# Kernel optimization log

Hardware: AMD Instinct MI355X
Metric: run time of the kernel (lower is better)

## Reference

```python
import jax, jax.numpy as jnp
import numpy as np
import math

D_MODEL = 1024
NUM_HEADS = 16
DK = D_MODEL // NUM_HEADS
THETA = 10000.0


def _rope(x, cos, sin):
    # x: (..., S, dk); cos/sin: (S, dk//2). Interleaved (even/odd) rotation,
    # matching x1=x[...,0::2], x2=x[...,1::2] then re-interleave via stack.
    x1 = x[..., 0::2]
    x2 = x[..., 1::2]
    r1 = x1 * cos - x2 * sin
    r2 = x1 * sin + x2 * cos
    return jnp.stack((r1, r2), axis=-1).reshape(x.shape)


def setup_inputs() -> dict:
    key = jax.random.key(0)
    k1, k2, k3 = jax.random.split(key, 3)
    B, S = 2, 2048
    x = jax.random.normal(k1, (B, S, D_MODEL), dtype=jnp.float32)
    std_qkv = (2.0 / (D_MODEL + 3 * D_MODEL)) ** 0.5
    Wqkv = jax.random.normal(k2, (3 * D_MODEL, D_MODEL), dtype=jnp.float32) * std_qkv
    std_o = (2.0 / (D_MODEL + D_MODEL)) ** 0.5
    Wo = jax.random.normal(k3, (D_MODEL, D_MODEL), dtype=jnp.float32) * std_o
    return {"x": x, "Wqkv": Wqkv, "Wo": Wo}


def reference(x, Wqkv, Wo):
    B, S, D = x.shape
    # fused QKV projection: Linear stores W as (out, in), y = x @ W^T
    qkv = jnp.einsum('bsd,od->bso', x, Wqkv)  # (B, S, 3*D)
    # split order in the source rearrange is (three, numheads, dk)
    qkv = qkv.reshape(B, S, 3, NUM_HEADS, DK).transpose(2, 0, 3, 1, 4)  # (3,B,H,S,dk)
    q, k, v = qkv[0], qkv[1], qkv[2]

    # RoPE tables (registered buffers in the source, deterministic constants)
    inv_freqs = 1.0 / (THETA ** (jnp.arange(0, DK, 2, dtype=jnp.float32) / DK))
    t = jnp.arange(S, dtype=jnp.float32)
    freqs = t[:, None] * inv_freqs[None, :]  # (S, dk//2)
    cos, sin = jnp.cos(freqs), jnp.sin(freqs)
    q = _rope(q, cos, sin)
    k = _rope(k, cos, sin)

    # naive full-materialization causal attention
    scores = jnp.einsum('bhqd,bhkd->bhqk', q, k) / math.sqrt(DK)  # (B,H,S,S)
    causal = jnp.tril(jnp.ones((S, S), dtype=bool))
    scores = jnp.where(causal, scores, -jnp.inf)
    attn = jax.nn.softmax(scores, axis=-1)
    out = jnp.einsum('bhqk,bhkd->bhqd', attn, v)  # (B,H,S,dk)
    out = out.transpose(0, 2, 1, 3).reshape(B, S, D)  # concat heads
    return jnp.einsum('bsd,od->bso', out, Wo)
```

## Files before the change

kernel.cpp:

```cpp
#include <hip/hip_runtime.h>
#include <hip/hip_bf16.h>
#include <cstdint>
#include <cstddef>


typedef unsigned short u16;
typedef unsigned int   u32;

typedef float f32x4 __attribute__((ext_vector_type(4)));
typedef short frag_t __attribute__((ext_vector_type(8)));

__device__ __forceinline__ f32x4 mfma16(frag_t a, frag_t b, f32x4 c) {
  return __builtin_amdgcn_mfma_f32_16x16x32_bf16(a, b, c, 0, 0, 0);
}

typedef __attribute__((address_space(1))) void as1_void;
typedef __attribute__((address_space(3))) void as3_void;
__device__ __forceinline__ void gload_lds16(const void* g, void* l) {
  __builtin_amdgcn_global_load_lds((as1_void*)g, (as3_void*)l, 16, 0, 0);
}

__device__ __forceinline__ u16 f2bf(float f) {
  u32 u = __builtin_bit_cast(u32, f);
  u += 0x7fffu + ((u >> 16) & 1u);
  return (u16)(u >> 16);
}
__device__ __forceinline__ float bf2f(u16 h) {
  u32 u = ((u32)h) << 16;
  return __builtin_bit_cast(float, u);
}
__device__ __forceinline__ u16 bf16u(float f) {
  __hip_bfloat16 h = __float2bfloat16(f);
  u16 u;
  __builtin_memcpy(&u, &h, 2);
  return u;
}
__device__ __forceinline__ float exp2_hw(float x) {
  float r;
  asm("v_exp_f32 %0, %1" : "=v"(r) : "v"(x));
  return r;
}
__device__ __forceinline__ void schedb() { __builtin_amdgcn_sched_barrier(0); }

static constexpr int Bb = 2, Ss = 2048, Hh = 16, Dd = 1024;
static constexpr int Mm = Bb * Ss;
static constexpr int NT = Ss / 64;

__global__ __launch_bounds__(256) void prep_kernel(const float* __restrict__ x,
                                                   const float* __restrict__ wqkv,
                                                   const float* __restrict__ wo,
                                                   u16* __restrict__ xb,
                                                   u16* __restrict__ wqkvb,
                                                   u16* __restrict__ wob,
                                                   float2* __restrict__ tab) {
  const int bid = blockIdx.x, tid = threadIdx.x;

  if (bid < 256) {
    const int i = bid * 256 + tid;
    const int s = i >> 5, j = i & 31;
    const float log2_theta_over_32 = 0.41524101186091903f;
    float inv = exp2f(-(float)j * log2_theta_over_32);
    float fr = (float)s * inv;
    float sn, cs;
    sincosf(fr, &sn, &cs);
    tab[i] = make_float2(cs, sn);
  }

  const int N1 = Mm * Dd / 4;
  const int N2 = N1 + 3 * Dd * Dd / 4;
  const int N3 = N2 + Dd * Dd / 4;
  for (int idx = bid * 256 + tid; idx < N3; idx += gridDim.x * 256) {
    const float4* src;
    u16* dst;
    int off;
    if (idx < N1)      { src = (const float4*)x;    dst = xb;    off = idx; }
    else if (idx < N2) { src = (const float4*)wqkv; dst = wqkvb; off = idx - N1; }
    else               { src = (const float4*)wo;   dst = wob;   off = idx - N2; }
    float4 v = src[off];
    ushort4 o;
    o.x = f2bf(v.x); o.y = f2bf(v.y); o.z = f2bf(v.z); o.w = f2bf(v.w);
    ((ushort4*)dst)[off] = o;
  }
}

__global__ __launch_bounds__(512, 2) void gemm8_kernel(const u16* __restrict__ A,
                                                       const u16* __restrict__ Bm,
                                                       u16* __restrict__ C,
                                                       int Mdim, int Ndim, int Kdim) {
  extern __shared__ __align__(16) u16 smem[];
  u16* As0 = smem;
  u16* As1 = smem + 16384;
  u16* Bs0 = smem + 32768;
  u16* Bs1 = smem + 49152;

  const int tid = threadIdx.x;
  const int lane = tid & 63, wid = tid >> 6;
  const int wr = wid >> 2, wc = wid & 3;
  const int lr = lane & 15, lg = lane >> 4;
  const int swk = lr & 7;

  const int nwg = gridDim.x * gridDim.y;
  const int orig = blockIdx.y * gridDim.x + blockIdx.x;
  const int cpx = nwg >> 3;
  const int swz = (orig & 7) * cpx + (orig >> 3);
  const int bx = swz % gridDim.x, by = swz / gridDim.x;
  const int m0 = by * 256, n0 = bx * 256;

  f32x4 acc[8][4] = {};

  const int strow = tid >> 3;
  const int sgr = tid & 7;

  auto stage_half = [&](u16* region, const u16* src, int grow0, int kt) {
#pragma unroll
    for (int rnd = 0; rnd < 2; rnd++) {
      const int lrow = rnd * 64 + strow;
      const u16* g = src + (size_t)(grow0 + lrow) * Kdim + kt * 64 +
                     ((sgr ^ (lrow & 7)) * 8);
      gload_lds16(g, region + (rnd * 64 + wid * 8) * 64);
    }
  };

  const int NK = Kdim >> 6;

  stage_half(As0, A, m0, 0);         stage_half(As0 + 8192, A, m0 + 128, 0);
  stage_half(Bs0, Bm, n0, 0);        stage_half(Bs0 + 8192, Bm, n0 + 128, 0);
  stage_half(Bs1, Bm, n0, 1);        stage_half(Bs1 + 8192, Bm, n0 + 128, 1);
  stage_half(As1, A, m0, 1);         stage_half(As1 + 8192, A, m0 + 128, 1);
  asm volatile("s_waitcnt vmcnt(8)" ::: "memory");
  schedb();
  __builtin_amdgcn_s_barrier();
  schedb();

  for (int kt = 0; kt < NK; kt++) {
    u16* Acur = (kt & 1) ? As1 : As0;
    u16* Bcur = (kt & 1) ? Bs1 : Bs0;
    const bool more = (kt + 2 < NK);
    frag_t bfr[4][2];

#pragma unroll
    for (int q = 0; q < 4; q++) {
      frag_t a[2][2];
#pragma unroll
      for (int mm = 0; mm < 2; mm++)
#pragma unroll
        for (int ks = 0; ks < 2; ks++)
          a[mm][ks] = *(const frag_t*)&Acur[(wr * 128 + (q * 2 + mm) * 16 + lr) * 64 +
                                            (((ks * 4 + lg) ^ swk) * 8)];
      if (q == 0) {
#pragma unroll
        for (int nt = 0; nt < 4; nt++)
#pragma unroll
          for (int ks = 0; ks < 2; ks++)
            bfr[nt][ks] = *(const frag_t*)&Bcur[(wc * 64 + nt * 16 + lr) * 64 +
                                                (((ks * 4 + lg) ^ swk) * 8)];
      }
      if (q == 1 && more) stage_half(Bcur, Bm, n0, kt + 2);
      if (q == 2 && more) stage_half(Bcur + 8192, Bm, n0 + 128, kt + 2);

      schedb();
      __builtin_amdgcn_s_barrier();
      schedb();
      __builtin_amdgcn_s_setprio(1);
#pragma unroll
      for (int ks = 0; ks < 2; ks++)
#pragma unroll
        for (int mm = 0; mm < 2; mm++)
#pragma unroll
          for (int nt = 0; nt < 4; nt++)
            acc[q * 2 + mm][nt] = mfma16(a[mm][ks], bfr[nt][ks], acc[q * 2 + mm][nt]);
      __builtin_amdgcn_s_setprio(0);
      __builtin_amdgcn_s_barrier();
      schedb();
    }

    if (kt + 1 < NK) {
      if (more) {
        stage_half(Acur, A, m0, kt + 2);
        stage_half(Acur + 8192, A, m0 + 128, kt + 2);
        asm volatile("s_waitcnt vmcnt(8)" ::: "memory");
      } else {
        asm volatile("s_waitcnt vmcnt(0)" ::: "memory");
      }
      schedb();
      __builtin_amdgcn_s_barrier();
      schedb();
    }
  }

#pragma unroll
  for (int m = 0; m < 8; m++)
#pragma unroll
    for (int n = 0; n < 4; n++)
#pragma unroll
      for (int r = 0; r < 4; r++) {
        size_t row = (size_t)(m0 + wr * 128 + m * 16 + lg * 4 + r);
        size_t col = (size_t)(n0 + wc * 64 + n * 16 + lr);
        C[row * Ndim + col] = f2bf(acc[m][n][r]);
      }
}

__global__ __launch_bounds__(256) void gemm_bt_kernel(const u16* __restrict__ A,
                                                      const u16* __restrict__ Bm,
                                                      float* __restrict__ Cv,
                                                      int Mdim, int Ndim, int Kdim) {
  __shared__ __align__(16) u16 As[2][128 * 64];
  __shared__ __align__(16) u16 Bs[2][128 * 64];
  const int tid = threadIdx.x;
  const int lane = tid & 63, wid = tid >> 6;
  const int wr = wid >> 1, wc = wid & 1;
  const int lr = lane & 15, lg = lane >> 4;

  const int nwg = gridDim.x * gridDim.y;
  const int orig = blockIdx.y * gridDim.x + blockIdx.x;
  const int cpx = nwg >> 3;
  const int swz = (orig & 7) * cpx + (orig >> 3);
  const int bx = swz % gridDim.x, by = swz / gridDim.x;
  const int m0 = by * 128, n0 = bx * 128;

  f32x4 acc[4][4] = {};

  const int rowA = lane >> 3;
  const int colu = ((lane & 7) ^ rowA) * 8;

  auto stage = [&](int buf, int kt) {
#pragma unroll
    for (int i = 0; i < 4; i++) {
      int chunk = wid * 4 + i;
      const u16* ga = A + (size_t)(m0 + chunk * 8 + rowA) * Kdim + kt + colu;
      gload_lds16(ga, &As[buf][chunk * 512]);
      const u16* gb = Bm + (size_t)(n0 + chunk * 8 + rowA) * Kdim + kt + colu;
      gload_lds16(gb, &Bs[buf][chunk * 512]);
    }
  };

  const int niter = Kdim >> 6;

  stage(0, 0);
  stage(1, 64);
  asm volatile("s_waitcnt vmcnt(8)" ::: "memory");
  schedb();
  __builtin_amdgcn_s_barrier();
  schedb();

  const int rsw = (lr & 7) * 8;
  int cur = 0;
  for (int it = 0; it < niter; ++it) {
#pragma unroll
    for (int ks = 0; ks < 2; ks++) {
      frag_t a[4], b[4];
#pragma unroll
      for (int mt = 0; mt < 4; mt++)
        a[mt] = *(const frag_t*)&As[cur][(wr * 64 + mt * 16 + lr) * 64 +
                                         ((ks * 32 + lg * 8) ^ rsw)];
#pragma unroll
      for (int nt = 0; nt < 4; nt++)
        b[nt] = *(const frag_t*)&Bs[cur][(wc * 64 + nt * 16 + lr) * 64 +
                                         ((ks * 32 + lg * 8) ^ rsw)];
#pragma unroll
      for (int mt = 0; mt < 4; mt++)
#pragma unroll
        for (int nt = 0; nt < 4; nt++)
          acc[mt][nt] = mfma16(a[mt], b[nt], acc[mt][nt]);
    }

    if (it + 1 < niter) {
      __builtin_amdgcn_s_barrier();
      schedb();
      if (it + 2 < niter) {
        stage(cur, (it + 2) << 6);
        asm volatile("s_waitcnt vmcnt(8)" ::: "memory");
      } else {
        asm volatile("s_waitcnt vmcnt(0)" ::: "memory");
      }
      schedb();
      __builtin_amdgcn_s_barrier();
      schedb();
      cur ^= 1;
    }
  }

#pragma unroll
  for (int mt = 0; mt < 4; mt++)
#pragma unroll
    for (int nt = 0; nt < 4; nt++)
#pragma unroll
      for (int r = 0; r < 4; r++) {
        size_t row = (size_t)(m0 + wr * 64 + mt * 16 + lg * 4 + r);
        size_t col = (size_t)(n0 + wc * 64 + nt * 16 + lr);
        Cv[row * Ndim + col] = acc[mt][nt][r];
      }
}

__global__ __launch_bounds__(256) void rope_kernel(const u16* __restrict__ qkv,
                                                   const float2* __restrict__ tab,
                                                   u16* __restrict__ q_r,
                                                   u16* __restrict__ k_r,
                                                   u16* __restrict__ vt) {
  const int bh = blockIdx.y, b = bh >> 4, h = bh & 15;
  const int s0 = blockIdx.x * 64;
  const int t = threadIdx.x;
  __shared__ __align__(16) u16 Vls[64 * 72];

  const int srow = t >> 2, c4 = t & 3;
  const int s = s0 + srow;
  const size_t rowbase = (size_t)(b * Ss + s) * 3072 + h * 64 + c4 * 16;

  u16 xq[16] __attribute__((aligned(16)));
  u16 xk[16] __attribute__((aligned(16)));
  u16 xv[16] __attribute__((aligned(16)));
  *(uint4*)&xq[0] = *(const uint4*)(qkv + rowbase);
  *(uint4*)&xq[8] = *(const uint4*)(qkv + rowbase + 8);
  *(uint4*)&xk[0] = *(const uint4*)(qkv + rowbase + 1024);
  *(uint4*)&xk[8] = *(const uint4*)(qkv + rowbase + 1024 + 8);
  *(uint4*)&xv[0] = *(const uint4*)(qkv + rowbase + 2048);
  *(uint4*)&xv[8] = *(const uint4*)(qkv + rowbase + 2048 + 8);

  u16 oq[16] __attribute__((aligned(16)));
  u16 ok[16] __attribute__((aligned(16)));
  const int j0 = c4 * 8;
  const float qscale = 0.125f * 1.4426950408889634f;
#pragma unroll
  for (int p = 0; p < 8; p++) {
    float2 cs = tab[s * 32 + j0 + p];
    float q1 = bf2f(xq[2 * p]), q2 = bf2f(xq[2 * p + 1]);
    float k1 = bf2f(xk[2 * p]), k2 = bf2f(xk[2 * p + 1]);
    oq[2 * p]     = f2bf((q1 * cs.x - q2 * cs.y) * qscale);
    oq[2 * p + 1] = f2bf((q1 * cs.y + q2 * cs.x) * qscale);
    ok[2 * p]     = f2bf(k1 * cs.x - k2 * cs.y);
    ok[2 * p + 1] = f2bf(k1 * cs.y + k2 * cs.x);
  }
  const size_t obase = ((size_t)bh * Ss + s) * 64 + c4 * 16;
  *(uint4*)(q_r + obase)     = *(uint4*)&oq[0];
  *(uint4*)(q_r + obase + 8) = *(uint4*)&oq[8];
  *(uint4*)(k_r + obase)     = *(uint4*)&ok[0];
  *(uint4*)(k_r + obase + 8) = *(uint4*)&ok[8];

  *(uint4*)&Vls[srow * 72 + c4 * 16]     = *(uint4*)&xv[0];
  *(uint4*)&Vls[srow * 72 + c4 * 16 + 8] = *(uint4*)&xv[8];
  __syncthreads();
  const int d = t >> 2, cq = t & 3;
  u16 ov[16] __attribute__((aligned(16)));
#pragma unroll
  for (int i = 0; i < 16; i++) ov[i] = Vls[(cq * 16 + i) * 72 + d];
  const size_t vbase = ((size_t)bh * 64 + d) * Ss + s0 + cq * 16;
  *(uint4*)(vt + vbase)     = *(uint4*)&ov[0];
  *(uint4*)(vt + vbase + 8) = *(uint4*)&ov[8];
}

__global__ __launch_bounds__(512, 4) void attn_kernel(const u16* __restrict__ q_r,
                                                      const u16* __restrict__ k_r,
                                                      const u16* __restrict__ vt,
                                                      u16* __restrict__ o) {
  const int pr = blockIdx.x;
  const int bh = blockIdx.y;
  const int b = bh >> 4, h = bh & 15;
  const int tid = threadIdx.x;
  const int lane = tid & 63, w = tid >> 6;
  const int ww = w & 3;
  const int lr = lane & 15, lg = lane >> 4;

  const int qt = (w < 4) ? pr : (NT - 1 - pr);
  const int qtB = NT - 1 - pr;

  __shared__ __align__(16) u16 Ks[2][64 * 64];
  __shared__ __align__(16) u16 Vs[2][64 * 64];
  __shared__ __align__(16) u16 Ps[8][16 * 64];

  const size_t kvbase = (size_t)bh * Ss * 64;
  const size_t vtbase = (size_t)bh * 64 * Ss;
  u16* Pw = &Ps[w][0];
  const int qrow = ww * 16 + lr;
  const int sw = lr & 7;

  frag_t q0f, q1f;
  {
    const u16* qa = q_r + kvbase + (size_t)(qt * 64 + qrow) * 64 + lg * 8;
    q0f = *(const frag_t*)qa;
    q1f = *(const frag_t*)(qa + 32);
  }

  const int srow = tid >> 3, sgr = tid & 7;
  const int scolg = sgr * 8;
  const int scols = (sgr ^ (srow & 7)) * 8;
  uint4 kreg, vreg;
  const u16* kp = k_r + kvbase;
  const u16* vp = vt + vtbase;

  auto issue = [&](int kt) {
    kreg = *(const uint4*)(kp + (size_t)(kt * 64 + srow) * 64 + scolg);
    vreg = *(const uint4*)(vp + (size_t)srow * Ss + kt * 64 + scolg);
  };
  auto commit = [&](int buf) {
    *(uint4*)&Ks[buf][srow * 64 + scols] = kreg;
    *(uint4*)&Vs[buf][srow * 64 + scols] = vreg;
  };

  f32x4 oacc[4] = {};
  float l_run = 0.f;

  issue(0);
  commit(0);
  __syncthreads();

  for (int kt = 0; kt <= qtB; kt++) {
    const int cur = kt & 1;
    const bool last = (kt == qtB);
    if (!last) issue(kt + 1);

    if (kt <= qt) {
      f32x4 sa[4];
      __builtin_amdgcn_s_setprio(1);
#pragma unroll
      for (int kf = 0; kf < 4; kf++) {
        frag_t k0 = *(const frag_t*)&Ks[cur][(kf * 16 + lr) * 64 + ((lg ^ sw) * 8)];
        frag_t k1 = *(const frag_t*)&Ks[cur][(kf * 16 + lr) * 64 + (((4 + lg) ^ sw) * 8)];
        sa[kf] = mfma16(k0, q0f, f32x4{0.f, 0.f, 0.f, 0.f});
        sa[kf] = mfma16(k1, q1f, sa[kf]);
      }
      __builtin_amdgcn_s_setprio(0);

      if (kt == qt) {
#pragma unroll
        for (int kf = 0; kf < 4; kf++)
#pragma unroll
          for (int r = 0; r < 4; r++)
            if (kf * 16 + lg * 4 + r > qrow) sa[kf][r] = -1e30f;
      }

      float ls = 0.f;
#pragma unroll
      for (int kf = 0; kf < 4; kf++) {
        float p0 = exp2_hw(sa[kf][0]), p1 = exp2_hw(sa[kf][1]);
        float p2 = exp2_hw(sa[kf][2]), p3 = exp2_hw(sa[kf][3]);
        ls += (p0 + p1) + (p2 + p3);
        ushort4 w4;
        w4.x = bf16u(p0); w4.y = bf16u(p1); w4.z = bf16u(p2); w4.w = bf16u(p3);
        const int pg = (kf * 2 + (lg >> 1)) ^ sw;
        *(ushort4*)&Pw[lr * 64 + pg * 8 + (lg & 1) * 4] = w4;
      }
      l_run += ls;

      __builtin_amdgcn_s_setprio(1);
#pragma unroll
      for (int ks = 0; ks < 2; ks++) {
        frag_t pa = *(const frag_t*)&Pw[lr * 64 + (((ks * 4 + lg) ^ sw) * 8)];
#pragma unroll
        for (int df = 0; df < 4; df++) {
          frag_t bv = *(const frag_t*)&Vs[cur][(df * 16 + lr) * 64 +
                                               (((ks * 4 + lg) ^ sw) * 8)];
          oacc[df] = mfma16(pa, bv, oacc[df]);
        }
      }
      __builtin_amdgcn_s_setprio(0);
    }

    if (!last) commit(cur ^ 1);
    __syncthreads();
  }

  l_run += __shfl_xor(l_run, 16);
  l_run += __shfl_xor(l_run, 32);
#pragma unroll
  for (int r = 0; r < 4; r++) {
    float il = 1.0f / __shfl(l_run, lg * 4 + r);
    size_t row = (size_t)b * Ss + qt * 64 + ww * 16 + lg * 4 + r;
#pragma unroll
    for (int df = 0; df < 4; df++)
      o[row * 1024 + h * 64 + df * 16 + lr] = f2bf(oacc[df][r] * il);
  }
}

extern "C" void kernel_launch(void* const* d_in, const int* in_sizes, int n_in,
                              void* d_out, int out_size, void* d_ws, size_t ws_size,
                              hipStream_t stream) {
  const float* x    = (const float*)d_in[0];
  const float* Wqkv = (const float*)d_in[1];
  const float* Wo   = (const float*)d_in[2];
  float* out = (float*)d_out;
  char* ws = (char*)d_ws;

  constexpr size_t TAB_OFF  = 0;
  constexpr size_t XB_OFF   = TAB_OFF + 524288;
  constexpr size_t WQB_OFF  = XB_OFF + 8388608;
  constexpr size_t WOB_OFF  = WQB_OFF + 6291456;
  constexpr size_t QKV_OFF  = WOB_OFF + 2097152;
  constexpr size_t QR_OFF   = QKV_OFF + 25165824;
  constexpr size_t KR_OFF   = QR_OFF + 8388608;
  constexpr size_t VT_OFF   = KR_OFF + 8388608;
  constexpr size_t AO_OFF   = VT_OFF + 8388608;

  float2* tab = (float2*)(ws + TAB_OFF);
  u16* xb     = (u16*)(ws + XB_OFF);
  u16* wqkvb  = (u16*)(ws + WQB_OFF);
  u16* wob    = (u16*)(ws + WOB_OFF);
  u16* qkv    = (u16*)(ws + QKV_OFF);
  u16* q_r    = (u16*)(ws + QR_OFF);
  u16* k_r    = (u16*)(ws + KR_OFF);
  u16* vt     = (u16*)(ws + VT_OFF);
  u16* ao     = (u16*)(ws + AO_OFF);

  prep_kernel<<<2048, 256, 0, stream>>>(x, Wqkv, Wo, xb, wqkvb, wob, tab);

  (void)hipFuncSetAttribute((const void*)gemm8_kernel,
                            hipFuncAttributeMaxDynamicSharedMemorySize, 131072);

  gemm8_kernel<<<dim3(3 * Dd / 256, Mm / 256), 512, 131072, stream>>>(
      xb, wqkvb, qkv, Mm, 3 * Dd, Dd);

  rope_kernel<<<dim3(Ss / 64, Bb * Hh), 256, 0, stream>>>(qkv, tab, q_r, k_r, vt);

  attn_kernel<<<dim3(NT / 2, Bb * Hh), 512, 0, stream>>>(q_r, k_r, vt, ao);

  gemm_bt_kernel<<<dim3(Dd / 128, Mm / 128), 256, 0, stream>>>(
      ao, wob, out, Mm, Dd, Dd);
}
```

Baseline: 117.4 us.

## Triple-buffer K/V in attention and software-pipeline QK^T one tile ahead

Moves the attention kernel's shared memory to a dynamic allocation with three K and V buffers. QK^T for tile kt+1 is computed while softmax and PV run for tile kt, and global loads are issued two tiles ahead. The aim is to overlap MFMA work with exp/LDS work and hide global load latency. In exchange it uses 64KB of LDS per block instead of 48KB, which may reduce occupancy, and it keeps extra score registers live.

```diff
diff --git a/kernel.cpp b/kernel.cpp
--- a/kernel.cpp
+++ b/kernel.cpp
@@ -352,6 +352,7 @@
                                                       const u16* __restrict__ k_r,
                                                       const u16* __restrict__ vt,
                                                       u16* __restrict__ o) {
+  extern __shared__ __align__(16) u16 asmem[];
   const int pr = blockIdx.x;
   const int bh = blockIdx.y;
   const int b = bh >> 4, h = bh & 15;
@@ -363,13 +364,10 @@
   const int qt = (w < 4) ? pr : (NT - 1 - pr);
   const int qtB = NT - 1 - pr;
 
-  __shared__ __align__(16) u16 Ks[2][64 * 64];
-  __shared__ __align__(16) u16 Vs[2][64 * 64];
-  __shared__ __align__(16) u16 Ps[8][16 * 64];
+  u16* Pw = asmem + 24576 + w * 1024;
 
   const size_t kvbase = (size_t)bh * Ss * 64;
   const size_t vtbase = (size_t)bh * 64 * Ss;
-  u16* Pw = &Ps[w][0];
   const int qrow = ww * 16 + lr;
   const int sw = lr & 7;
 
@@ -392,47 +390,58 @@
     vreg = *(const uint4*)(vp + (size_t)srow * Ss + kt * 64 + scolg);
   };
   auto commit = [&](int buf) {
-    *(uint4*)&Ks[buf][srow * 64 + scols] = kreg;
-    *(uint4*)&Vs[buf][srow * 64 + scols] = vreg;
+    *(uint4*)&asmem[buf * 4096 + srow * 64 + scols] = kreg;
+    *(uint4*)&asmem[12288 + buf * 4096 + srow * 64 + scols] = vreg;
+  };
+
+  auto qk_compute = [&](int buf, f32x4* sa) {
+    const u16* Kb = asmem + buf * 4096;
+    __builtin_amdgcn_s_setprio(1);
+#pragma unroll
+    for (int kf = 0; kf < 4; kf++) {
+      frag_t k0 = *(const frag_t*)&Kb[(kf * 16 + lr) * 64 + ((lg ^ sw) * 8)];
+      frag_t k1 = *(const frag_t*)&Kb[(kf * 16 + lr) * 64 + (((4 + lg) ^ sw) * 8)];
+      sa[kf] = mfma16(k0, q0f, f32x4{0.f, 0.f, 0.f, 0.f});
+      sa[kf] = mfma16(k1, q1f, sa[kf]);
+    }
+    __builtin_amdgcn_s_setprio(0);
   };
 
   f32x4 oacc[4] = {};
   float l_run = 0.f;
+  f32x4 saP[4];
 
   issue(0);
   commit(0);
   __syncthreads();
+  qk_compute(0, saP);
+  issue(1);
+  commit(1);
+  __syncthreads();
+  issue(2);
 
   for (int kt = 0; kt <= qtB; kt++) {
-    const int cur = kt & 1;
-    const bool last = (kt == qtB);
-    if (!last) issue(kt + 1);
+    const int bP = kt % 3, bN = (kt + 1) % 3, bC = (kt + 2) % 3;
+
+    if (kt + 2 <= qtB) commit(bC);
+
+    f32x4 saN[4];
+    if (kt + 1 <= qt) qk_compute(bN, saN);
 
     if (kt <= qt) {
-      f32x4 sa[4];
-      __builtin_amdgcn_s_setprio(1);
+      if (kt == qt) {
+#pragma unroll
+        for (int kf = 0; kf < 4; kf++)
+#pragma unroll
+          for (int r = 0; r < 4; r++)
+            if (kf * 16 + lg * 4 + r > qrow) saP[kf][r] = -1e30f;
+      }
+
+      float ls = 0.f;
 #pragma unroll
       for (int kf = 0; kf < 4; kf++) {
-        frag_t k0 = *(const frag_t*)&Ks[cur][(kf * 16 + lr) * 64 + ((lg ^ sw) * 8)];
-        frag_t k1 = *(const frag_t*)&Ks[cur][(kf * 16 + lr) * 64 + (((4 + lg) ^ sw) * 8)];
-        sa[kf] = mfma16(k0, q0f, f32x4{0.f, 0.f, 0.f, 0.f});
-        sa[kf] = mfma16(k1, q1f, sa[kf]);
-      }
-      __builtin_amdgcn_s_setprio(0);
-
-      if (kt == qt) {
-#pragma unroll
-        for (int kf = 0; kf < 4; kf++)
-#pragma unroll
-          for (int r = 0; r < 4; r++)
-            if (kf * 16 + lg * 4 + r > qrow) sa[kf][r] = -1e30f;
-      }
-
-      float ls = 0.f;
-#pragma unroll
-      for (int kf = 0; kf < 4; kf++) {
-        float p0 = exp2_hw(sa[kf][0]), p1 = exp2_hw(sa[kf][1]);
-        float p2 = exp2_hw(sa[kf][2]), p3 = exp2_hw(sa[kf][3]);
+        float p0 = exp2_hw(saP[kf][0]), p1 = exp2_hw(saP[kf][1]);
+        float p2 = exp2_hw(saP[kf][2]), p3 = exp2_hw(saP[kf][3]);
         ls += (p0 + p1) + (p2 + p3);
         ushort4 w4;
         w4.x = bf16u(p0); w4.y = bf16u(p1); w4.z = bf16u(p2); w4.w = bf16u(p3);
@@ -441,21 +450,25 @@
       }
       l_run += ls;
 
+      const u16* Vb = asmem + 12288 + bP * 4096;
       __builtin_amdgcn_s_setprio(1);
 #pragma unroll
       for (int ks = 0; ks < 2; ks++) {
         frag_t pa = *(const frag_t*)&Pw[lr * 64 + (((ks * 4 + lg) ^ sw) * 8)];
 #pragma unroll
         for (int df = 0; df < 4; df++) {
-          frag_t bv = *(const frag_t*)&Vs[cur][(df * 16 + lr) * 64 +
-                                               (((ks * 4 + lg) ^ sw) * 8)];
+          frag_t bv = *(const frag_t*)&Vb[(df * 16 + lr) * 64 +
+                                          (((ks * 4 + lg) ^ sw) * 8)];
           oacc[df] = mfma16(pa, bv, oacc[df]);
         }
       }
       __builtin_amdgcn_s_setprio(0);
     }
 
-    if (!last) commit(cur ^ 1);
+    if (kt + 3 <= qtB) issue(kt + 3);
+
+#pragma unroll
+    for (int i = 0; i < 4; i++) saP[i] = saN[i];
     __syncthreads();
   }
 
@@ -504,13 +517,15 @@
 
   (void)hipFuncSetAttribute((const void*)gemm8_kernel,
                             hipFuncAttributeMaxDynamicSharedMemorySize, 131072);
+  (void)hipFuncSetAttribute((const void*)attn_kernel,
+                            hipFuncAttributeMaxDynamicSharedMemorySize, 65536);
 
   gemm8_kernel<<<dim3(3 * Dd / 256, Mm / 256), 512, 131072, stream>>>(
       xb, wqkvb, qkv, Mm, 3 * Dd, Dd);
 
   rope_kernel<<<dim3(Ss / 64, Bb * Hh), 256, 0, stream>>>(qkv, tab, q_r, k_r, vt);
 
-  attn_kernel<<<dim3(NT / 2, Bb * Hh), 512, 0, stream>>>(q_r, k_r, vt, ao);
+  attn_kernel<<<dim3(NT / 2, Bb * Hh), 512, 65536, stream>>>(q_r, k_r, vt, ao);
 
   gemm_bt_kernel<<<dim3(Dd / 128, Mm / 128), 256, 0, stream>>>(
       ao, wob, out, Mm, Dd, Dd);
```

Result: no change. 116.7 us, median of 3 (-0.6%).
